# Kernel optimization log

Measured on AMD Instinct MI355X. Metric: run time of the kernel, lower is better.

Reference implementation:

```python
import jax, jax.numpy as jnp
import numpy as np

DIM, D_INNER, D_STATE, DT_RANK, D_CONV = 1024, 2048, 16, 64, 4
BATCH, SEQ = 2, 1024

def setup_inputs() -> dict:
    key = jax.random.key(0)
    ks = jax.random.split(key, 9)
    s = 0.02
    A = jnp.tile(jnp.arange(1, D_STATE + 1, dtype=jnp.float32), (D_INNER, 1))
    return {
        "x": jax.random.normal(ks[0], (BATCH, SEQ, DIM), jnp.float32),
        "in_proj_w": jax.random.normal(ks[1], (DIM, 2 * D_INNER), jnp.float32) * s,
        "conv_w": jax.random.normal(ks[2], (D_INNER, 1, D_CONV), jnp.float32) * 0.2,
        "conv_b": jax.random.normal(ks[3], (D_INNER,), jnp.float32) * 0.1,
        "x_proj_w": jax.random.normal(ks[4], (D_INNER, DT_RANK + 2 * D_STATE), jnp.float32) * s,
        "dt_proj_w": jax.random.normal(ks[5], (DT_RANK, D_INNER), jnp.float32) * s,
        "dt_proj_b": jax.random.normal(ks[6], (D_INNER,), jnp.float32) * 0.1,
        "A_log": jnp.log(A),
        "D_param": jnp.ones((D_INNER,), jnp.float32),
        "out_proj_w": jax.random.normal(ks[7], (D_INNER, DIM), jnp.float32) * s,
    }

def _silu(v):
    return v * jax.nn.sigmoid(v)

def _ssm_forward(x, in_proj_w, conv_w, conv_b, x_proj_w, dt_proj_w, dt_proj_b, A_log, D_param, out_proj_w):
    b, l, _ = x.shape
    d_inner, d_conv = conv_w.shape[0], conv_w.shape[2]
    dt_rank, n = dt_proj_w.shape[0], A_log.shape[1]
    # input projection and split into conv branch / gate branch
    x_and_res = x @ in_proj_w                      # (b, l, 2*d_inner)
    xp, res = x_and_res[..., :d_inner], x_and_res[..., d_inner:]
    # causal depthwise conv (torch pads d_conv-1 both sides then slices [:l])
    h = jax.lax.conv_general_dilated(
        xp.transpose(0, 2, 1), conv_w,
        window_strides=(1,), padding=[(d_conv - 1, 0)],
        dimension_numbers=("NCH", "OIH", "NCH"),
        feature_group_count=d_inner,
    ) + conv_b[None, :, None]                      # (b, d_inner, l)
    h = _silu(h.transpose(0, 2, 1))                # (b, l, d_inner)
    # input-dependent SSM parameters
    A = -jnp.exp(A_log)                            # (d_inner, n)
    x_dbl = h @ x_proj_w                           # (b, l, dt_rank + 2n)
    dlt, Bm, Cm = (x_dbl[..., :dt_rank],
                   x_dbl[..., dt_rank:dt_rank + n],
                   x_dbl[..., dt_rank + n:])
    delta = jax.nn.softplus(dlt @ dt_proj_w + dt_proj_b)   # (b, l, d_inner)
    # discretization
    deltaA = jnp.exp(jnp.einsum("bld,dn->bldn", delta, A))             # (b,l,d,n)
    deltaB_u = (delta * h)[..., None] * Bm[:, :, None, :]              # (b,l,d,n)
    # sequential selective scan over time via lax.scan
    def step(state, t):
        dA_t, dBu_t, c_t = t
        state = dA_t * state + dBu_t               # (b, d, n)
        y_t = jnp.einsum("bdn,bn->bd", state, c_t)
        return state, y_t
    init = jnp.zeros((b, d_inner, n), h.dtype)
    _, ys = jax.lax.scan(step, init,
                         (deltaA.transpose(1, 0, 2, 3),
                          deltaB_u.transpose(1, 0, 2, 3),
                          Cm.transpose(1, 0, 2)))
    y = ys.transpose(1, 0, 2) + h * D_param        # (b, l, d_inner)
    y = y * _silu(res)
    return y @ out_proj_w                          # (b, l, dim)

def reference(x, in_proj_w, conv_w, conv_b, x_proj_w, dt_proj_w, dt_proj_b, A_log, D_param, out_proj_w):
    return _ssm_forward(x, in_proj_w, conv_w, conv_b, x_proj_w, dt_proj_w, dt_proj_b, A_log, D_param, out_proj_w)
```

## Files before the change

### kernel.cpp

```cpp
#include <hip/hip_runtime.h>
#include <hip/hip_bf16.h>

#define DIM     1024
#define DINNER  2048
#define NSTATE  16
#define DTRANK  64
#define DCONV   4
#define BATCH   2
#define SEQ     1024
#define BL      (BATCH*SEQ)
#define XDBLW   96
#define NCHUNK  32
#define TCHUNK  32
#define KSLICE  16
#define G4SK    4
#define LOG2E   1.44269504088896f
#define LN2     0.69314718055995f

typedef __attribute__((ext_vector_type(4))) float  f32x4;
typedef __attribute__((ext_vector_type(8))) short  bf16x8;
typedef unsigned short ushort_t;

__device__ __forceinline__ ushort_t f2bf(float f) {
    union { float f; unsigned int u; } v; v.f = f;
    unsigned int lsb = (v.u >> 16) & 1u;
    v.u += 0x7fffu + lsb;
    return (ushort_t)(v.u >> 16);
}
__device__ __forceinline__ float bf2f(ushort_t h) {
    union { unsigned u; float f; } v; v.u = ((unsigned)h) << 16; return v.f;
}
__device__ __forceinline__ float hexp2(float x) { return __builtin_amdgcn_exp2f(x); }
__device__ __forceinline__ float hlog2(float x) { return __builtin_amdgcn_logf(x); }
__device__ __forceinline__ float hrcp(float x)  { return __builtin_amdgcn_rcpf(x); }
__device__ __forceinline__ float softplus_fast(float x) {
    float e = hexp2(-fabsf(x) * LOG2E);
    return fmaxf(x, 0.f) + LN2 * hlog2(1.f + e);
}
__device__ __forceinline__ float sigmoid_fast(float x) {
    return hrcp(1.f + hexp2(-x * LOG2E));
}

typedef __attribute__((address_space(1))) unsigned int gu32_t;
typedef __attribute__((address_space(3))) unsigned int lu32_t;
__device__ __forceinline__ void gload_lds16(const ushort_t* g, ushort_t* l) {
    __builtin_amdgcn_global_load_lds((const gu32_t*)(const void*)g,
                                     (lu32_t*)(void*)l, 16, 0, 0);
}

__global__ __launch_bounds__(256) void prep_fused(
    const float* __restrict__ Win,  ushort_t* __restrict__ WtIn,
    const float* __restrict__ Wout, ushort_t* __restrict__ WtOut,
    const float* __restrict__ Wxp,  ushort_t* __restrict__ WtXp,
    const float* __restrict__ x,    ushort_t* __restrict__ xb)
{
    __shared__ float tile[32][33];
    const int tid = threadIdx.x;
    const int tx = tid & 31, ty = tid >> 5;
    const int bid = blockIdx.x;

    const float* src; ushort_t* dst; int R, C, bx, by;
    if (bid < 4096)      { src = Win;  dst = WtIn;  R = 1024; C = 4096; int j = bid;        bx = j % 128; by = j / 128; }
    else if (bid < 6144) { src = Wout; dst = WtOut; R = 2048; C = 1024; int j = bid - 4096; bx = j % 32;  by = j / 32; }
    else if (bid < 6336) { src = Wxp;  dst = WtXp;  R = 2048; C = 96;   int j = bid - 6144; bx = j % 3;   by = j / 3; }
    else {
        int i = ((bid - 6336) * 256 + tid) * 4;
        f32x4 v = *(const f32x4*)(x + i);
        ushort_t r0 = f2bf(v[0]), r1 = f2bf(v[1]), r2 = f2bf(v[2]), r3 = f2bf(v[3]);
        *(uint2*)(xb + i) = make_uint2((unsigned)r0 | ((unsigned)r1 << 16),
                                       (unsigned)r2 | ((unsigned)r3 << 16));
        return;
    }

    const int r0 = by * 32, c0 = bx * 32;
    #pragma unroll
    for (int i = 0; i < 4; ++i)
        tile[ty + i * 8][tx] = src[(size_t)(r0 + ty + i * 8) * C + c0 + tx];
    __syncthreads();
    #pragma unroll
    for (int i = 0; i < 4; ++i)
        dst[(size_t)(c0 + ty + i * 8) * R + r0 + tx] = f2bf(tile[tx][ty + i * 8]);
}

__global__ __launch_bounds__(512) void gemm_lds(
    const ushort_t* __restrict__ A,  int lda,
    const ushort_t* __restrict__ Bt, int ldb,
    int K,
    float* __restrict__ Cf, ushort_t* __restrict__ Cb, int ldc)
{
    __shared__ ushort_t As[2][128 * 64];
    __shared__ ushort_t Bs[2][128 * 64];

    const int tid  = threadIdx.x;
    const int m0   = blockIdx.y * 128;
    const int n0   = blockIdx.x * 128;
    const int wid  = tid >> 6;
    const int lane = tid & 63;
    const int wm   = (wid >> 2) * 64;
    const int wn   = (wid & 3) * 32;
    const int lr   = lane & 15;

    int rq[2], gq[2], lo[2];
    #pragma unroll
    for (int q = 0; q < 2; ++q) {
        int c = q * 512 + tid;
        rq[q] = c >> 3;
        gq[q] = ((c & 7) ^ (rq[q] & 7)) * 8;
        lo[q] = (q * 512 + wid * 64) * 8;
    }

    f32x4 acc[4][2];
    #pragma unroll
    for (int m = 0; m < 4; ++m)
        #pragma unroll
        for (int n = 0; n < 2; ++n)
            acc[m][n] = (f32x4){0.f, 0.f, 0.f, 0.f};

    const int nk = K >> 6;

    #pragma unroll
    for (int q = 0; q < 2; ++q) {
        gload_lds16(A  + (size_t)(m0 + rq[q]) * lda + gq[q], &As[0][lo[q]]);
        gload_lds16(Bt + (size_t)(n0 + rq[q]) * ldb + gq[q], &Bs[0][lo[q]]);
    }

    for (int k = 0; k < nk; ++k) {
        const int cur = k & 1;
        if (k + 1 < nk) {
            const int k0 = (k + 1) << 6;
            #pragma unroll
            for (int q = 0; q < 2; ++q) {
                gload_lds16(A  + (size_t)(m0 + rq[q]) * lda + k0 + gq[q], &As[cur ^ 1][lo[q]]);
                gload_lds16(Bt + (size_t)(n0 + rq[q]) * ldb + k0 + gq[q], &Bs[cur ^ 1][lo[q]]);
            }
            asm volatile("s_waitcnt vmcnt(4)" ::: "memory");
        } else {
            asm volatile("s_waitcnt vmcnt(0)" ::: "memory");
        }
        __builtin_amdgcn_sched_barrier(0);
        __builtin_amdgcn_s_barrier();

        #pragma unroll
        for (int kk = 0; kk < 2; ++kk) {
            const int lg = (lane >> 4) + kk * 4;
            const int pc = (lg ^ (lr & 7)) * 8;
            bf16x8 af[4], bfr[2];
            #pragma unroll
            for (int m = 0; m < 4; ++m)
                af[m] = *(const bf16x8*)(&As[cur][(wm + m * 16 + lr) * 64 + pc]);
            #pragma unroll
            for (int n = 0; n < 2; ++n)
                bfr[n] = *(const bf16x8*)(&Bs[cur][(wn + n * 16 + lr) * 64 + pc]);
            #pragma unroll
            for (int m = 0; m < 4; ++m)
                #pragma unroll
                for (int n = 0; n < 2; ++n)
                    acc[m][n] = __builtin_amdgcn_mfma_f32_16x16x32_bf16(af[m], bfr[n], acc[m][n], 0, 0, 0);
        }
        __builtin_amdgcn_s_barrier();
    }

    const int rbase = (lane >> 4) * 4;
    #pragma unroll
    for (int m = 0; m < 4; ++m) {
        #pragma unroll
        for (int n = 0; n < 2; ++n) {
            int col = n0 + wn + n * 16 + lr;
            #pragma unroll
            for (int r = 0; r < 4; ++r) {
                int row = m0 + wm + m * 16 + rbase + r;
                float v = acc[m][n][r];
                if (Cf) Cf[(size_t)row * ldc + col] = v;
                if (Cb) Cb[(size_t)row * ldc + col] = f2bf(v);
            }
        }
    }
}

__global__ __launch_bounds__(512) void gemm_lds_sk(
    const ushort_t* __restrict__ A,  int lda,
    const ushort_t* __restrict__ Bt, int ldb,
    int klen,
    float* __restrict__ Part, int ldc, int mn)
{
    __shared__ ushort_t As[2][128 * 64];
    __shared__ ushort_t Bs[2][128 * 64];

    const int tid  = threadIdx.x;
    const int m0   = blockIdx.y * 128;
    const int n0   = blockIdx.x * 128;
    const int kb   = blockIdx.z * klen;
    float* Cf = Part + (size_t)blockIdx.z * mn;

    const int wid  = tid >> 6;
    const int lane = tid & 63;
    const int wm   = (wid >> 2) * 64;
    const int wn   = (wid & 3) * 32;
    const int lr   = lane & 15;

    int rq[2], gq[2], lo[2];
    #pragma unroll
    for (int q = 0; q < 2; ++q) {
        int c = q * 512 + tid;
        rq[q] = c >> 3;
        gq[q] = ((c & 7) ^ (rq[q] & 7)) * 8;
        lo[q] = (q * 512 + wid * 64) * 8;
    }

    f32x4 acc[4][2];
    #pragma unroll
    for (int m = 0; m < 4; ++m)
        #pragma unroll
        for (int n = 0; n < 2; ++n)
            acc[m][n] = (f32x4){0.f, 0.f, 0.f, 0.f};

    const int nk = klen >> 6;

    #pragma unroll
    for (int q = 0; q < 2; ++q) {
        gload_lds16(A  + (size_t)(m0 + rq[q]) * lda + kb + gq[q], &As[0][lo[q]]);
        gload_lds16(Bt + (size_t)(n0 + rq[q]) * ldb + kb + gq[q], &Bs[0][lo[q]]);
    }

    for (int k = 0; k < nk; ++k) {
        const int cur = k & 1;
        if (k + 1 < nk) {
            const int k0 = kb + ((k + 1) << 6);
            #pragma unroll
            for (int q = 0; q < 2; ++q) {
                gload_lds16(A  + (size_t)(m0 + rq[q]) * lda + k0 + gq[q], &As[cur ^ 1][lo[q]]);
                gload_lds16(Bt + (size_t)(n0 + rq[q]) * ldb + k0 + gq[q], &Bs[cur ^ 1][lo[q]]);
            }
            asm volatile("s_waitcnt vmcnt(4)" ::: "memory");
        } else {
            asm volatile("s_waitcnt vmcnt(0)" ::: "memory");
        }
        __builtin_amdgcn_sched_barrier(0);
        __builtin_amdgcn_s_barrier();

        #pragma unroll
        for (int kk = 0; kk < 2; ++kk) {
            const int lg = (lane >> 4) + kk * 4;
            const int pc = (lg ^ (lr & 7)) * 8;
            bf16x8 af[4], bfr[2];
            #pragma unroll
            for (int m = 0; m < 4; ++m)
                af[m] = *(const bf16x8*)(&As[cur][(wm + m * 16 + lr) * 64 + pc]);
            #pragma unroll
            for (int n = 0; n < 2; ++n)
                bfr[n] = *(const bf16x8*)(&Bs[cur][(wn + n * 16 + lr) * 64 + pc]);
            #pragma unroll
            for (int m = 0; m < 4; ++m)
                #pragma unroll
                for (int n = 0; n < 2; ++n)
                    acc[m][n] = __builtin_amdgcn_mfma_f32_16x16x32_bf16(af[m], bfr[n], acc[m][n], 0, 0, 0);
        }
        __builtin_amdgcn_s_barrier();
    }

    const int rbase = (lane >> 4) * 4;
    #pragma unroll
    for (int m = 0; m < 4; ++m) {
        #pragma unroll
        for (int n = 0; n < 2; ++n) {
            int col = n0 + wn + n * 16 + lr;
            #pragma unroll
            for (int r = 0; r < 4; ++r) {
                int row = m0 + wm + m * 16 + rbase + r;
                Cf[(size_t)row * ldc + col] = acc[m][n][r];
            }
        }
    }
}

__global__ __launch_bounds__(256) void g4_reduce(
    const float* __restrict__ Part, float* __restrict__ out)
{
    int i = (blockIdx.x * 256 + threadIdx.x) * 4;
    const size_t mn = (size_t)BL * DIM;
    f32x4 s = *(const f32x4*)(Part + i);
    #pragma unroll
    for (int z = 1; z < G4SK; ++z)
        s += *(const f32x4*)(Part + z * mn + i);
    *(f32x4*)(out + i) = s;
}

__global__ __launch_bounds__(256) void gemm_n96_splitk(
    const ushort_t* __restrict__ A,
    const ushort_t* __restrict__ Bt,
    float* __restrict__ Ppart)
{
    __shared__ ushort_t As[128 * 40];
    __shared__ ushort_t Bs[96 * 40];

    const int tid   = threadIdx.x;
    const int ks    = blockIdx.x;
    const int m0    = blockIdx.y * 128;
    const int kbase = ks * (DINNER / KSLICE);
    const int wid   = tid >> 6;
    const int lane  = tid & 63;
    const int wm    = wid * 32;
    const int lr    = lane & 15;
    const int lk    = (lane >> 4) * 8;

    f32x4 acc[2][6];
    #pragma unroll
    for (int m = 0; m < 2; ++m)
        #pragma unroll
        for (int n = 0; n < 6; ++n)
            acc[m][n] = (f32x4){0.f, 0.f, 0.f, 0.f};

    for (int k0 = kbase; k0 < kbase + DINNER / KSLICE; k0 += 32) {
        #pragma unroll
        for (int c = 0; c < 2; ++c) {
            int cid = tid + c * 256;
            int row = cid >> 2, ck = (cid & 3) * 8;
            *(uint4*)(&As[row * 40 + ck]) =
                *(const uint4*)(A + (size_t)(m0 + row) * DINNER + k0 + ck);
        }
        {
            int row = tid >> 2, ck = (tid & 3) * 8;
            *(uint4*)(&Bs[row * 40 + ck]) =
                *(const uint4*)(Bt + (size_t)row * DINNER + k0 + ck);
            if (tid < 128) {
                int cid = 256 + tid;
                int row2 = cid >> 2, ck2 = (cid & 3) * 8;
                *(uint4*)(&Bs[row2 * 40 + ck2]) =
                    *(const uint4*)(Bt + (size_t)row2 * DINNER + k0 + ck2);
            }
        }
        __syncthreads();

        bf16x8 af[2], bfr[6];
        #pragma unroll
        for (int m = 0; m < 2; ++m)
            af[m] = *(const bf16x8*)(&As[(wm + m * 16 + lr) * 40 + lk]);
        #pragma unroll
        for (int n = 0; n < 6; ++n)
            bfr[n] = *(const bf16x8*)(&Bs[(n * 16 + lr) * 40 + lk]);

        #pragma unroll
        for (int m = 0; m < 2; ++m)
            #pragma unroll
            for (int n = 0; n < 6; ++n)
                acc[m][n] = __builtin_amdgcn_mfma_f32_16x16x32_bf16(af[m], bfr[n], acc[m][n], 0, 0, 0);
        __syncthreads();
    }

    const int rbase = (lane >> 4) * 4;
    #pragma unroll
    for (int m = 0; m < 2; ++m) {
        #pragma unroll
        for (int n = 0; n < 6; ++n) {
            int col = n * 16 + lr;
            #pragma unroll
            for (int r = 0; r < 4; ++r) {
                int row = m0 + wm + m * 16 + rbase + r;
                Ppart[((size_t)ks * BL + row) * XDBLW + col] = acc[m][n][r];
            }
        }
    }
}

__global__ __launch_bounds__(256) void g2_reduce(
    const float* __restrict__ Ppart, float* __restrict__ xdbl)
{
    int idx = blockIdx.x * 256 + threadIdx.x;
    int row = idx / 24, cg = (idx % 24) * 4;
    f32x4 s = (f32x4){0.f, 0.f, 0.f, 0.f};
    #pragma unroll
    for (int ks = 0; ks < KSLICE; ++ks)
        s += *(const f32x4*)(Ppart + ((size_t)ks * BL + row) * XDBLW + cg);
    *(f32x4*)(xdbl + (size_t)row * XDBLW + cg) = s;
}

__global__ __launch_bounds__(256, 4) void delta_v6(
    const float* __restrict__ xdbl,
    const float* __restrict__ Wdt,
    const float* __restrict__ dtb,
    ushort_t* __restrict__ delta_bf)
{
    __shared__ float WS[64][256];
    __shared__ float dS[32][64];
    const int tid  = threadIdx.x;
    const int d0   = (blockIdx.x & 7) * 256;
    const int row0 = (blockIdx.x >> 3) * 32;

    #pragma unroll
    for (int i = 0; i < 16; ++i) {
        int c = i * 256 + tid;
        int k = c >> 6, co = (c & 63) * 4;
        *(f32x4*)&WS[k][co] = *(const f32x4*)(Wdt + (size_t)k * DINNER + d0 + co);
    }
    #pragma unroll
    for (int i = 0; i < 2; ++i) {
        int c = i * 256 + tid;
        int r = c >> 4, co = (c & 15) * 4;
        *(f32x4*)&dS[r][co] = *(const f32x4*)(xdbl + (size_t)(row0 + r) * XDBLW + co);
    }
    __syncthreads();

    const int w    = tid >> 6;
    const int lane = tid & 63;
    const int dd   = lane * 4;

    f32x4 acc[8];
    {
        f32x4 bb = *(const f32x4*)(dtb + d0 + dd);
        #pragma unroll
        for (int r = 0; r < 8; ++r) acc[r] = bb;
    }

    for (int kq = 0; kq < 16; ++kq) {
        f32x4 dv[8];
        #pragma unroll
        for (int r = 0; r < 8; ++r)
            dv[r] = *(const f32x4*)&dS[w * 8 + r][kq * 4];
        #pragma unroll
        for (int kk = 0; kk < 4; ++kk) {
            f32x4 wv = *(const f32x4*)&WS[kq * 4 + kk][dd];
            #pragma unroll
            for (int r = 0; r < 8; ++r) {
                float dk = dv[r][kk];
                acc[r][0] = fmaf(dk, wv[0], acc[r][0]);
                acc[r][1] = fmaf(dk, wv[1], acc[r][1]);
                acc[r][2] = fmaf(dk, wv[2], acc[r][2]);
                acc[r][3] = fmaf(dk, wv[3], acc[r][3]);
            }
        }
    }

    #pragma unroll
    for (int r = 0; r < 8; ++r) {
        const size_t rowb = (size_t)(row0 + w * 8 + r) * DINNER + d0;
        f32x4 v = acc[r];
        ushort_t o[4];
        #pragma unroll
        for (int j = 0; j < 4; ++j)
            o[j] = f2bf(softplus_fast(v[j]));
        *(uint2*)(delta_bf + rowb + dd) = make_uint2(
            (unsigned)o[0] | ((unsigned)o[1] << 16), (unsigned)o[2] | ((unsigned)o[3] << 16));
    }
}

__global__ __launch_bounds__(256) void conv_silu(
    const ushort_t* __restrict__ xrb,
    const float* __restrict__ convw,
    const float* __restrict__ convb,
    ushort_t* __restrict__ hb)
{
    const int bt = blockIdx.x;
    const int t  = bt & (SEQ - 1);
    const int d0 = threadIdx.x * 8;

    bf16x8 xv[DCONV];
    #pragma unroll
    for (int j = 0; j < DCONV; ++j) {
        int tt = t + j - (DCONV - 1);
        if (tt >= 0)
            xv[j] = *(const bf16x8*)(xrb + (size_t)(bt + j - (DCONV - 1)) * 4096 + d0);
        else
            xv[j] = (bf16x8){0,0,0,0,0,0,0,0};
    }

    ushort_t o[8];
    #pragma unroll
    for (int dd = 0; dd < 8; ++dd) {
        f32x4 w = *(const f32x4*)(convw + (size_t)(d0 + dd) * DCONV);
        float acc = convb[d0 + dd];
        #pragma unroll
        for (int j = 0; j < DCONV; ++j)
            acc = fmaf(w[j], bf2f((ushort_t)xv[j][dd]), acc);
        o[dd] = f2bf(acc * sigmoid_fast(acc));
    }
    uint4 pk;
    pk.x = (unsigned)o[0] | ((unsigned)o[1] << 16);
    pk.y = (unsigned)o[2] | ((unsigned)o[3] << 16);
    pk.z = (unsigned)o[4] | ((unsigned)o[5] << 16);
    pk.w = (unsigned)o[6] | ((unsigned)o[7] << 16);
    *(uint4*)(hb + (size_t)bt * DINNER + d0) = pk;
}

__global__ __launch_bounds__(256) void scan_p1(
    const ushort_t* __restrict__ delta_bf,
    const ushort_t* __restrict__ hb,
    const float* __restrict__ xdbl,
    const float* __restrict__ Alog,
    float* __restrict__ Pbuf,
    float* __restrict__ Sbuf)
{
    const int d  = (blockIdx.x & 7) * 256 + threadIdx.x;
    const int bc = blockIdx.x >> 3;
    const int b  = bc >> 5;
    const int c  = bc & (NCHUNK - 1);
    const int t0 = c * TCHUNK;

    float A[NSTATE];
    #pragma unroll
    for (int q = 0; q < 4; ++q) {
        f32x4 al = *(const f32x4*)(Alog + (size_t)d * NSTATE + q * 4);
        #pragma unroll
        for (int j = 0; j < 4; ++j)
            A[q * 4 + j] = -hexp2(al[j] * LOG2E) * LOG2E;
    }

    float s[NSTATE], pp[NSTATE];
    #pragma unroll
    for (int n = 0; n < NSTATE; ++n) { s[n] = 0.f; pp[n] = 1.f; }

    for (int tt = 0; tt < TCHUNK; ++tt) {
        const size_t row = (size_t)(b * SEQ + t0 + tt);
        float dl = bf2f(delta_bf[row * DINNER + d]);
        float hv = bf2f(hb[row * DINNER + d]);
        float dlh = dl * hv;
        float Bv[NSTATE];
        #pragma unroll
        for (int q = 0; q < 4; ++q) {
            f32x4 bv = *(const f32x4*)(xdbl + row * XDBLW + DTRANK + q * 4);
            #pragma unroll
            for (int j = 0; j < 4; ++j) Bv[q * 4 + j] = bv[j];
        }
        #pragma unroll
        for (int n = 0; n < NSTATE; ++n) {
            float a = hexp2(dl * A[n]);
            s[n]  = fmaf(a, s[n], dlh * Bv[n]);
            pp[n] *= a;
        }
    }

    const size_t o = (((size_t)b * NCHUNK + c) * DINNER + d) * NSTATE;
    #pragma unroll
    for (int q = 0; q < 4; ++q) {
        *(f32x4*)(Sbuf + o + q * 4) = (f32x4){s[q*4+0], s[q*4+1], s[q*4+2], s[q*4+3]};
        *(f32x4*)(Pbuf + o + q * 4) = (f32x4){pp[q*4+0], pp[q*4+1], pp[q*4+2], pp[q*4+3]};
    }
}

__global__ __launch_bounds__(256) void scan_p2(
    const float* __restrict__ Pbuf, float* __restrict__ Sbuf)
{
    const int tid = blockIdx.x * 256 + threadIdx.x;
    const int n = tid & 15;
    const int d = (tid >> 4) & (DINNER - 1);
    const int b = tid >> 15;
    const size_t stride = (size_t)DINNER * NSTATE;
    const size_t base = ((size_t)b * NCHUNK * DINNER + d) * NSTATE + n;

    float S[NCHUNK], P[NCHUNK];
    #pragma unroll
    for (int c = 0; c < NCHUNK; ++c) {
        S[c] = Sbuf[base + c * stride];
        P[c] = Pbuf[base + c * stride];
    }
    float cin = 0.f;
    float O[NCHUNK];
    #pragma unroll
    for (int c = 0; c < NCHUNK; ++c) {
        O[c] = cin;
        cin = fmaf(P[c], cin, S[c]);
    }
    #pragma unroll
    for (int c = 0; c < NCHUNK; ++c)
        Sbuf[base + c * stride] = O[c];
}

__global__ __launch_bounds__(256) void scan_p3(
    const ushort_t* __restrict__ delta_bf,
    const ushort_t* __restrict__ hb,
    const float* __restrict__ xdbl,
    const ushort_t* __restrict__ xrb,
    const float* __restrict__ Alog,
    const float* __restrict__ Dp,
    const float* __restrict__ Sbuf,
    ushort_t* __restrict__ yb)
{
    const int d  = (blockIdx.x & 7) * 256 + threadIdx.x;
    const int bc = blockIdx.x >> 3;
    const int b  = bc >> 5;
    const int c  = bc & (NCHUNK - 1);
    const int t0 = c * TCHUNK;

    float A[NSTATE];
    #pragma unroll
    for (int q = 0; q < 4; ++q) {
        f32x4 al = *(const f32x4*)(Alog + (size_t)d * NSTATE + q * 4);
        #pragma unroll
        for (int j = 0; j < 4; ++j)
            A[q * 4 + j] = -hexp2(al[j] * LOG2E) * LOG2E;
    }
    const float Dd = Dp[d];

    float s[NSTATE];
    const size_t o = (((size_t)b * NCHUNK + c) * DINNER + d) * NSTATE;
    #pragma unroll
    for (int q = 0; q < 4; ++q) {
        f32x4 sv = *(const f32x4*)(Sbuf + o + q * 4);
        #pragma unroll
        for (int j = 0; j < 4; ++j) s[q * 4 + j] = sv[j];
    }

    for (int tt = 0; tt < TCHUNK; ++tt) {
        const size_t row = (size_t)(b * SEQ + t0 + tt);
        float dl = bf2f(delta_bf[row * DINNER + d]);
        float hv = bf2f(hb[row * DINNER + d]);
        float rv = bf2f(xrb[row * 4096 + DINNER + d]);
        float dlh = dl * hv;
        float Bv[NSTATE], Cv[NSTATE];
        #pragma unroll
        for (int q = 0; q < 4; ++q) {
            f32x4 bv = *(const f32x4*)(xdbl + row * XDBLW + DTRANK + q * 4);
            f32x4 cv = *(const f32x4*)(xdbl + row * XDBLW + DTRANK + NSTATE + q * 4);
            #pragma unroll
            for (int j = 0; j < 4; ++j) { Bv[q*4+j] = bv[j]; Cv[q*4+j] = cv[j]; }
        }
        float y = 0.f;
        #pragma unroll
        for (int n = 0; n < NSTATE; ++n) {
            float a = hexp2(dl * A[n]);
            s[n] = fmaf(a, s[n], dlh * Bv[n]);
            y = fmaf(s[n], Cv[n], y);
        }
        y = fmaf(hv, Dd, y);
        y = y * rv * sigmoid_fast(rv);
        yb[row * DINNER + d] = f2bf(y);
    }
}

extern "C" void kernel_launch(void* const* d_in, const int* in_sizes, int n_in,
                              void* d_out, int out_size, void* d_ws, size_t ws_size,
                              hipStream_t stream)
{
    const float* x     = (const float*)d_in[0];
    const float* Win   = (const float*)d_in[1];
    const float* convw = (const float*)d_in[2];
    const float* convb = (const float*)d_in[3];
    const float* Wxp   = (const float*)d_in[4];
    const float* Wdt   = (const float*)d_in[5];
    const float* dtb   = (const float*)d_in[6];
    const float* Alog  = (const float*)d_in[7];
    const float* Dp    = (const float*)d_in[8];
    const float* Wout  = (const float*)d_in[9];
    float* out = (float*)d_out;

    char* base = (char*)d_ws; size_t off = 0;
    auto alloc = [&](size_t bytes) -> char* {
        char* q = base + off;
        off = (off + bytes + 255) & ~(size_t)255;
        return q;
    };
    ushort_t* WtIn   = (ushort_t*)alloc((size_t)4096 * 1024 * 2);
    ushort_t* WtOut  = (ushort_t*)alloc((size_t)1024 * 2048 * 2);
    ushort_t* WtXp   = (ushort_t*)alloc((size_t)96   * 2048 * 2);
    ushort_t* xb     = (ushort_t*)alloc((size_t)BL * DIM * 2);
    ushort_t* xrb    = (ushort_t*)alloc((size_t)BL * 4096 * 2);
    ushort_t* hb     = (ushort_t*)alloc((size_t)BL * DINNER * 2);
    float*    xdbl   = (float*)   alloc((size_t)BL * XDBLW * 4);
    ushort_t* dltbf  = (ushort_t*)alloc((size_t)BL * DINNER * 2);
    ushort_t* yb     = (ushort_t*)alloc((size_t)BL * DINNER * 2);
    float*    Pbuf   = (float*)   alloc((size_t)BATCH * NCHUNK * DINNER * NSTATE * 4);
    float*    Sbuf   = (float*)   alloc((size_t)BATCH * NCHUNK * DINNER * NSTATE * 4);
    float*    Ppart  = (float*)   alloc((size_t)KSLICE * BL * XDBLW * 4);
    float*    G4part = (float*)   alloc((size_t)G4SK * BL * DIM * 4);
    (void)ws_size;

    prep_fused<<<dim3(8384), 256, 0, stream>>>(Win, WtIn, Wout, WtOut, Wxp, WtXp, x, xb);

    gemm_lds<<<dim3(4096/128, BL/128), 512, 0, stream>>>(
        xb, DIM, WtIn, DIM, DIM, nullptr, xrb, 2*DINNER);

    conv_silu<<<dim3(BL), 256, 0, stream>>>(xrb, convw, convb, hb);

    gemm_n96_splitk<<<dim3(KSLICE, BL/128), 256, 0, stream>>>(hb, WtXp, Ppart);
    g2_reduce<<<dim3(BL * 24 / 256), 256, 0, stream>>>(Ppart, xdbl);

    delta_v6<<<dim3(8 * (BL / 32)), 256, 0, stream>>>(xdbl, Wdt, dtb, dltbf);

    scan_p1<<<dim3(8 * BATCH * NCHUNK), 256, 0, stream>>>(dltbf, hb, xdbl, Alog, Pbuf, Sbuf);
    scan_p2<<<dim3(BATCH * DINNER * NSTATE / 256), 256, 0, stream>>>(Pbuf, Sbuf);
    scan_p3<<<dim3(8 * BATCH * NCHUNK), 256, 0, stream>>>(dltbf, hb, xdbl, xrb, Alog, Dp, Sbuf, yb);

    gemm_lds_sk<<<dim3(DIM/128, BL/128, G4SK), 512, 0, stream>>>(
        yb, DINNER, WtOut, DINNER, DINNER/G4SK, G4part, DIM, BL*DIM);
    g4_reduce<<<dim3(BL*DIM/4/256), 256, 0, stream>>>(G4part, out);
}
```

Before: 139.7 us.

## Fuse delta projection into scan phase-1 kernel, staging delta in LDS

Merges the delta (dt_proj + softplus) kernel into the first chunked-scan kernel, so each block computes delta for its 32-row chunk and stages it in shared memory before running the intra-chunk scan. This removes one launch and the global re-read of delta in phase 1. Delta is still written to global memory for phase 3. The dt_proj weights are now kept in LDS as bf16 to fit the shared buffer, which adds unpack work and some rounding.

```diff
diff --git a/kernel.cpp b/kernel.cpp
--- a/kernel.cpp
+++ b/kernel.cpp
@@ -30,6 +30,11 @@
 __device__ __forceinline__ float bf2f(ushort_t h) {
     union { unsigned u; float f; } v; v.u = ((unsigned)h) << 16; return v.f;
 }
+__device__ __forceinline__ void unpack_bf2(unsigned u, float& lo, float& hi) {
+    union { unsigned x; float f; } a, b;
+    a.x = u << 16; b.x = u & 0xffff0000u;
+    lo = a.f; hi = b.f;
+}
 __device__ __forceinline__ float hexp2(float x) { return __builtin_amdgcn_exp2f(x); }
 __device__ __forceinline__ float hlog2(float x) { return __builtin_amdgcn_logf(x); }
 __device__ __forceinline__ float hrcp(float x)  { return __builtin_amdgcn_rcpf(x); }
@@ -374,29 +379,43 @@
     *(f32x4*)(xdbl + (size_t)row * XDBLW + cg) = s;
 }
 
-__global__ __launch_bounds__(256, 4) void delta_v6(
+__global__ __launch_bounds__(256, 4) void scan_p1f(
     const float* __restrict__ xdbl,
     const float* __restrict__ Wdt,
     const float* __restrict__ dtb,
-    ushort_t* __restrict__ delta_bf)
-{
-    __shared__ float WS[64][256];
-    __shared__ float dS[32][64];
-    const int tid  = threadIdx.x;
-    const int d0   = (blockIdx.x & 7) * 256;
-    const int row0 = (blockIdx.x >> 3) * 32;
+    const ushort_t* __restrict__ hb,
+    const float* __restrict__ Alog,
+    ushort_t* __restrict__ delta_bf,
+    float* __restrict__ Pbuf,
+    float* __restrict__ Sbuf)
+{
+    __shared__ __align__(16) char smem[40960];
+    ushort_t (*WSb)[256] = (ushort_t(*)[256])smem;
+    float    (*dlS)[256] = (float(*)[256])smem;
+    float    (*dS)[64]   = (float(*)[64])(smem + 32768);
+
+    const int tid = threadIdx.x;
+    const int d0  = (blockIdx.x & 7) * 256;
+    const int bc  = blockIdx.x >> 3;
+    const int b   = bc >> 5;
+    const int c   = bc & (NCHUNK - 1);
+    const int t0  = c * TCHUNK;
+    const size_t row0 = (size_t)(b * SEQ + t0);
 
     #pragma unroll
     for (int i = 0; i < 16; ++i) {
-        int c = i * 256 + tid;
-        int k = c >> 6, co = (c & 63) * 4;
-        *(f32x4*)&WS[k][co] = *(const f32x4*)(Wdt + (size_t)k * DINNER + d0 + co);
+        int cc = i * 256 + tid;
+        int k = cc >> 6, co = (cc & 63) * 4;
+        f32x4 v = *(const f32x4*)(Wdt + (size_t)k * DINNER + d0 + co);
+        ushort_t b0 = f2bf(v[0]), b1 = f2bf(v[1]), b2 = f2bf(v[2]), b3 = f2bf(v[3]);
+        *(uint2*)&WSb[k][co] = make_uint2((unsigned)b0 | ((unsigned)b1 << 16),
+                                          (unsigned)b2 | ((unsigned)b3 << 16));
     }
     #pragma unroll
     for (int i = 0; i < 2; ++i) {
-        int c = i * 256 + tid;
-        int r = c >> 4, co = (c & 15) * 4;
-        *(f32x4*)&dS[r][co] = *(const f32x4*)(xdbl + (size_t)(row0 + r) * XDBLW + co);
+        int cc = i * 256 + tid;
+        int r = cc >> 4, co = (cc & 15) * 4;
+        *(f32x4*)&dS[r][co] = *(const f32x4*)(xdbl + (row0 + r) * XDBLW + co);
     }
     __syncthreads();
 
@@ -410,7 +429,6 @@
         #pragma unroll
         for (int r = 0; r < 8; ++r) acc[r] = bb;
     }
-
     for (int kq = 0; kq < 16; ++kq) {
         f32x4 dv[8];
         #pragma unroll
@@ -418,28 +436,82 @@
             dv[r] = *(const f32x4*)&dS[w * 8 + r][kq * 4];
         #pragma unroll
         for (int kk = 0; kk < 4; ++kk) {
-            f32x4 wv = *(const f32x4*)&WS[kq * 4 + kk][dd];
+            uint2 wp = *(const uint2*)&WSb[kq * 4 + kk][dd];
+            float w0, w1, w2, w3;
+            unpack_bf2(wp.x, w0, w1);
+            unpack_bf2(wp.y, w2, w3);
             #pragma unroll
             for (int r = 0; r < 8; ++r) {
                 float dk = dv[r][kk];
-                acc[r][0] = fmaf(dk, wv[0], acc[r][0]);
-                acc[r][1] = fmaf(dk, wv[1], acc[r][1]);
-                acc[r][2] = fmaf(dk, wv[2], acc[r][2]);
-                acc[r][3] = fmaf(dk, wv[3], acc[r][3]);
+                acc[r][0] = fmaf(dk, w0, acc[r][0]);
+                acc[r][1] = fmaf(dk, w1, acc[r][1]);
+                acc[r][2] = fmaf(dk, w2, acc[r][2]);
+                acc[r][3] = fmaf(dk, w3, acc[r][3]);
             }
         }
     }
 
+    float rr[8][4];
     #pragma unroll
     for (int r = 0; r < 8; ++r) {
-        const size_t rowb = (size_t)(row0 + w * 8 + r) * DINNER + d0;
-        f32x4 v = acc[r];
         ushort_t o[4];
         #pragma unroll
-        for (int j = 0; j < 4; ++j)
-            o[j] = f2bf(softplus_fast(v[j]));
+        for (int j = 0; j < 4; ++j) {
+            float sp = softplus_fast(acc[r][j]);
+            o[j] = f2bf(sp);
+            rr[r][j] = bf2f(o[j]);
+        }
+        const size_t rowb = (row0 + w * 8 + r) * DINNER + d0;
         *(uint2*)(delta_bf + rowb + dd) = make_uint2(
             (unsigned)o[0] | ((unsigned)o[1] << 16), (unsigned)o[2] | ((unsigned)o[3] << 16));
+    }
+
+    __syncthreads();
+    #pragma unroll
+    for (int r = 0; r < 8; ++r)
+        *(f32x4*)&dlS[w * 8 + r][dd] = (f32x4){rr[r][0], rr[r][1], rr[r][2], rr[r][3]};
+    __syncthreads();
+
+    const int d = d0 + tid;
+
+    float A[NSTATE];
+    #pragma unroll
+    for (int q = 0; q < 4; ++q) {
+        f32x4 al = *(const f32x4*)(Alog + (size_t)d * NSTATE + q * 4);
+        #pragma unroll
+        for (int j = 0; j < 4; ++j)
+            A[q * 4 + j] = -hexp2(al[j] * LOG2E) * LOG2E;
+    }
+
+    float s[NSTATE], pp[NSTATE];
+    #pragma unroll
+    for (int n = 0; n < NSTATE; ++n) { s[n] = 0.f; pp[n] = 1.f; }
+
+    for (int tt = 0; tt < TCHUNK; ++tt) {
+        const size_t row = row0 + tt;
+        float dl = dlS[tt][tid];
+        float hv = bf2f(hb[row * DINNER + d]);
+        float dlh = dl * hv;
+        float Bv[NSTATE];
+        #pragma unroll
+        for (int q = 0; q < 4; ++q) {
+            f32x4 bv = *(const f32x4*)(xdbl + row * XDBLW + DTRANK + q * 4);
+            #pragma unroll
+            for (int j = 0; j < 4; ++j) Bv[q * 4 + j] = bv[j];
+        }
+        #pragma unroll
+        for (int n = 0; n < NSTATE; ++n) {
+            float a = hexp2(dl * A[n]);
+            s[n]  = fmaf(a, s[n], dlh * Bv[n]);
+            pp[n] *= a;
+        }
+    }
+
+    const size_t o = (((size_t)b * NCHUNK + c) * DINNER + d) * NSTATE;
+    #pragma unroll
+    for (int q = 0; q < 4; ++q) {
+        *(f32x4*)(Sbuf + o + q * 4) = (f32x4){s[q*4+0], s[q*4+1], s[q*4+2], s[q*4+3]};
+        *(f32x4*)(Pbuf + o + q * 4) = (f32x4){pp[q*4+0], pp[q*4+1], pp[q*4+2], pp[q*4+3]};
     }
 }
 
@@ -479,61 +551,6 @@
     pk.z = (unsigned)o[4] | ((unsigned)o[5] << 16);
     pk.w = (unsigned)o[6] | ((unsigned)o[7] << 16);
     *(uint4*)(hb + (size_t)bt * DINNER + d0) = pk;
-}
-
-__global__ __launch_bounds__(256) void scan_p1(
-    const ushort_t* __restrict__ delta_bf,
-    const ushort_t* __restrict__ hb,
-    const float* __restrict__ xdbl,
-    const float* __restrict__ Alog,
-    float* __restrict__ Pbuf,
-    float* __restrict__ Sbuf)
-{
-    const int d  = (blockIdx.x & 7) * 256 + threadIdx.x;
-    const int bc = blockIdx.x >> 3;
-    const int b  = bc >> 5;
-    const int c  = bc & (NCHUNK - 1);
-    const int t0 = c * TCHUNK;
-
-    float A[NSTATE];
-    #pragma unroll
-    for (int q = 0; q < 4; ++q) {
-        f32x4 al = *(const f32x4*)(Alog + (size_t)d * NSTATE + q * 4);
-        #pragma unroll
-        for (int j = 0; j < 4; ++j)
-            A[q * 4 + j] = -hexp2(al[j] * LOG2E) * LOG2E;
-    }
-
-    float s[NSTATE], pp[NSTATE];
-    #pragma unroll
-    for (int n = 0; n < NSTATE; ++n) { s[n] = 0.f; pp[n] = 1.f; }
-
-    for (int tt = 0; tt < TCHUNK; ++tt) {
-        const size_t row = (size_t)(b * SEQ + t0 + tt);
-        float dl = bf2f(delta_bf[row * DINNER + d]);
-        float hv = bf2f(hb[row * DINNER + d]);
-        float dlh = dl * hv;
-        float Bv[NSTATE];
-        #pragma unroll
-        for (int q = 0; q < 4; ++q) {
-            f32x4 bv = *(const f32x4*)(xdbl + row * XDBLW + DTRANK + q * 4);
-            #pragma unroll
-            for (int j = 0; j < 4; ++j) Bv[q * 4 + j] = bv[j];
-        }
-        #pragma unroll
-        for (int n = 0; n < NSTATE; ++n) {
-            float a = hexp2(dl * A[n]);
-            s[n]  = fmaf(a, s[n], dlh * Bv[n]);
-            pp[n] *= a;
-        }
-    }
-
-    const size_t o = (((size_t)b * NCHUNK + c) * DINNER + d) * NSTATE;
-    #pragma unroll
-    for (int q = 0; q < 4; ++q) {
-        *(f32x4*)(Sbuf + o + q * 4) = (f32x4){s[q*4+0], s[q*4+1], s[q*4+2], s[q*4+3]};
-        *(f32x4*)(Pbuf + o + q * 4) = (f32x4){pp[q*4+0], pp[q*4+1], pp[q*4+2], pp[q*4+3]};
-    }
 }
 
 __global__ __launch_bounds__(256) void scan_p2(
@@ -673,9 +690,9 @@
     gemm_n96_splitk<<<dim3(KSLICE, BL/128), 256, 0, stream>>>(hb, WtXp, Ppart);
     g2_reduce<<<dim3(BL * 24 / 256), 256, 0, stream>>>(Ppart, xdbl);
 
-    delta_v6<<<dim3(8 * (BL / 32)), 256, 0, stream>>>(xdbl, Wdt, dtb, dltbf);
-
-    scan_p1<<<dim3(8 * BATCH * NCHUNK), 256, 0, stream>>>(dltbf, hb, xdbl, Alog, Pbuf, Sbuf);
+    scan_p1f<<<dim3(8 * BATCH * NCHUNK), 256, 0, stream>>>(
+        xdbl, Wdt, dtb, hb, Alog, dltbf, Pbuf, Sbuf);
+
     scan_p2<<<dim3(BATCH * DINNER * NSTATE / 256), 256, 0, stream>>>(Pbuf, Sbuf);
     scan_p3<<<dim3(8 * BATCH * NCHUNK), 256, 0, stream>>>(dltbf, hb, xdbl, xrb, Alog, Dp, Sbuf, yb);
 
```

Result: no change. 138.8 us (-0.7%).
